# Kernel optimization log

Hardware: AMD Instinct MI355X
Metric: run time of the kernel (lower is better)

Reference implementation:

```python
import jax, jax.numpy as jnp
import numpy as np

E = 1024   # embed_dim
H = 16     # num_heads
D = E // H # head_dim = 64
HD2 = D // 2
B = 2
S = 2048


def setup_inputs() -> dict:
    key = jax.random.key(0)
    ks = jax.random.split(key, 12)
    def lin(k, fan_in, fan_out):
        # xavier-uniform-ish init, stored in [in, out] (jax) convention
        lim = float(np.sqrt(6.0 / (fan_in + fan_out)))
        return jax.random.uniform(k, (fan_in, fan_out), jnp.float32, -lim, lim)
    return {
        "query": jax.random.normal(ks[0], (B, S, E), jnp.float32),
        "xi_scale": jax.random.uniform(ks[1], (B,), jnp.float32),
        "Wq": lin(ks[2], E, E), "bq": jnp.zeros((E,), jnp.float32),
        "Wk": lin(ks[3], E, E), "bk": jnp.zeros((E,), jnp.float32),
        "Wv": lin(ks[4], E, E), "bv": jnp.zeros((E,), jnp.float32),
        "Wo": lin(ks[5], E, E), "bo": jnp.zeros((E,), jnp.float32),
        "enc_w1": lin(ks[6], 1, HD2), "enc_b1": jnp.zeros((HD2,), jnp.float32),
        "ln_g": jnp.ones((HD2,), jnp.float32), "ln_b": jnp.zeros((HD2,), jnp.float32),
        "enc_w2": lin(ks[7], HD2, D), "enc_b2": jnp.zeros((D,), jnp.float32),
        "scale_gating": jnp.ones((H,), jnp.float32),
    }


def reference(query, xi_scale, Wq, bq, Wk, bk, Wv, bv, Wo, bo,
              enc_w1, enc_b1, ln_g, ln_b, enc_w2, enc_b2, scale_gating):
    b, s, e = query.shape
    h, d = H, e // H
    # --- scale adaptation: xi -> Linear -> LayerNorm -> GELU -> Linear ---
    x = xi_scale[:, None] @ enc_w1 + enc_b1                  # [B, D/2]
    mu = x.mean(-1, keepdims=True)
    var = ((x - mu) ** 2).mean(-1, keepdims=True)
    x = (x - mu) / jnp.sqrt(var + 1e-5) * ln_g + ln_b
    x = jax.nn.gelu(x, approximate=False)
    xe = x @ enc_w2 + enc_b2                                 # [B, D]
    adapt = 1.0 + jax.nn.sigmoid(scale_gating)[None, :, None] * xe[:, None, :]  # [B, H, D]
    # --- projections (self-attention: key = value = query) ---
    q = (query @ Wq + bq).reshape(b, s, h, d).transpose(0, 2, 1, 3) * adapt[:, :, None, :]
    k = (query @ Wk + bk).reshape(b, s, h, d).transpose(0, 2, 1, 3) * adapt[:, :, None, :]
    v = (query @ Wv + bv).reshape(b, s, h, d).transpose(0, 2, 1, 3)
    # --- explicit QK^T / sqrt(d) -> softmax -> V ---
    inv_scale = 1.0 / float(np.sqrt(d))
    scores = jnp.einsum('bhqd,bhkd->bhqk', q, k) * inv_scale  # [B, H, S, S]
    attn = jax.nn.softmax(scores, axis=-1)
    out = jnp.einsum('bhqk,bhkd->bhqd', attn, v)              # [B, H, S, D]
    out = out.transpose(0, 2, 1, 3).reshape(b, s, e)
    return out @ Wo + bo
```

## Files before the change

### kernel.cpp

```cpp
#include <hip/hip_runtime.h>

typedef __bf16 bf16;
typedef __attribute__((ext_vector_type(8))) __bf16 bf16x8;
typedef __attribute__((ext_vector_type(4))) float f32x4;
typedef __attribute__((ext_vector_type(16))) float f32x16;
typedef unsigned int u32;

#define MFMA16(a, b, c) __builtin_amdgcn_mfma_f32_16x16x32_bf16((a), (b), (c), 0, 0, 0)
#define MFMA32(a, b, c) __builtin_amdgcn_mfma_f32_32x32x16_bf16((a), (b), (c), 0, 0, 0)

#define BB 2
#define SS 2048
#define EE 1024
#define HH 16
#define DD 64
#define MM (BB * SS)

__device__ inline f32x4 zero4() {
    f32x4 z; z.x = 0.f; z.y = 0.f; z.z = 0.f; z.w = 0.f; return z;
}

__device__ __forceinline__ void gload16(const bf16* g, bf16* l) {
    __builtin_amdgcn_global_load_lds(
        (const __attribute__((address_space(1))) u32*)(const void*)g,
        (__attribute__((address_space(3))) u32*)(void*)l,
        16, 0, 0);
}

__device__ __forceinline__ u32 pkbf(float a, float b) {
    union { __bf16 h; unsigned short s; } ua, ub;
    ua.h = (__bf16)a; ub.h = (__bf16)b;
    return (u32)ua.s | ((u32)ub.s << 16);
}

__global__ __launch_bounds__(256) void prep_kernel(
    const float* __restrict__ query, bf16* __restrict__ qc,
    const float* __restrict__ s0, const float* __restrict__ s1,
    const float* __restrict__ s2, const float* __restrict__ s3,
    bf16* __restrict__ d0, bf16* __restrict__ d1,
    bf16* __restrict__ d2, bf16* __restrict__ d3,
    const float* __restrict__ xi, const float* __restrict__ w1,
    const float* __restrict__ b1, const float* __restrict__ lng,
    const float* __restrict__ lnb, const float* __restrict__ w2,
    const float* __restrict__ b2, const float* __restrict__ gate,
    float* __restrict__ adapt) {
    __shared__ bf16 tile[64 * 72];
    const int bid = blockIdx.x;
    const int t = threadIdx.x;

    if (bid < 2048) {
        const int i = (bid * 256 + t) * 8;
        float4 a = *(const float4*)(query + i);
        float4 b = *(const float4*)(query + i + 4);
        bf16 tmp[8];
        tmp[0] = (bf16)a.x; tmp[1] = (bf16)a.y; tmp[2] = (bf16)a.z; tmp[3] = (bf16)a.w;
        tmp[4] = (bf16)b.x; tmp[5] = (bf16)b.y; tmp[6] = (bf16)b.z; tmp[7] = (bf16)b.w;
        *(uint4*)(qc + i) = *(uint4*)tmp;
    } else if (bid < 3072) {
        const int m = (bid - 2048) >> 8;
        const int idx0 = (bid - 2048) & 255;
        const float* W = (m == 0) ? s0 : (m == 1) ? s1 : (m == 2) ? s2 : s3;
        bf16* Wt = (m == 0) ? d0 : (m == 1) ? d1 : (m == 2) ? d2 : d3;
        const int k0 = (idx0 >> 4) * 64, n0 = (idx0 & 15) * 64;
#pragma unroll
        for (int i = 0; i < 2; ++i) {
            int idx = i * 256 + t;
            int r = idx >> 3, c = (idx & 7) * 8;
            float4 a = *(const float4*)(W + (k0 + r) * EE + n0 + c);
            float4 b = *(const float4*)(W + (k0 + r) * EE + n0 + c + 4);
            bf16 tmp[8];
            tmp[0] = (bf16)a.x; tmp[1] = (bf16)a.y; tmp[2] = (bf16)a.z; tmp[3] = (bf16)a.w;
            tmp[4] = (bf16)b.x; tmp[5] = (bf16)b.y; tmp[6] = (bf16)b.z; tmp[7] = (bf16)b.w;
            *(uint4*)(tile + r * 72 + c) = *(uint4*)tmp;
        }
        __syncthreads();
#pragma unroll
        for (int i = 0; i < 2; ++i) {
            int idx = i * 256 + t;
            int n = idx >> 3, kc = (idx & 7) * 8;
            bf16 tmp[8];
#pragma unroll
            for (int j = 0; j < 8; ++j) tmp[j] = tile[(kc + j) * 72 + n];
            *(uint4*)(Wt + (n0 + n) * EE + k0 + kc) = *(uint4*)tmp;
        }
    } else {
        const int b = bid - 3072;
        float* xs = (float*)tile;
        if (t < 64) {
            const float xiv = xi[b];
            float xv = 0.f;
            if (t < 32) xv = xiv * w1[t] + b1[t];
            float sm = xv;
            for (int off = 1; off < 32; off <<= 1) sm += __shfl_xor(sm, off);
            const float mu = sm * (1.f / 32.f);
            float dv = (t < 32) ? (xv - mu) : 0.f;
            float s2 = dv * dv;
            for (int off = 1; off < 32; off <<= 1) s2 += __shfl_xor(s2, off);
            const float var = s2 * (1.f / 32.f);
            if (t < 32) {
                float xn = (xv - mu) * rsqrtf(var + 1e-5f) * lng[t] + lnb[t];
                float ge = 0.5f * xn * (1.f + erff(xn * 0.70710678118654752f));
                xs[t] = ge;
            }
        }
        __syncthreads();
        if (t < 64) {
            float acc = b2[t];
            for (int j = 0; j < 32; ++j) acc += xs[j] * w2[j * DD + t];
            for (int h = 0; h < HH; ++h) {
                float sg = 1.f / (1.f + __expf(-gate[h]));
                adapt[(b * HH + h) * DD + t] = 1.f + sg * acc;
            }
        }
    }
}

__global__ __launch_bounds__(256, 3) void gemm_qkv(
    const bf16* __restrict__ Aq, const bf16* __restrict__ Bqk,
    const bf16* __restrict__ Av,
    const float* __restrict__ bias, const float* __restrict__ bias2,
    const float* __restrict__ bias3, const float* __restrict__ adapt,
    bf16* __restrict__ outqk, bf16* __restrict__ outvt) {
    __shared__ bf16 sh[16384];
    bf16* As = sh;
    bf16* Bs = sh + 8192;

    const int t = threadIdx.x;
    const int w = t >> 6, lane = t & 63;
    const int mrow = lane & 15, quad = lane >> 4;
    const int wm = (w & 1) * 64, wn = (w >> 1) * 64;

    int md, bx, by;
    const bf16 *Ap, *Bp;
    int bid = blockIdx.x;
    if (bid < 512) { md = 5; bx = bid & 31; by = bid >> 5; Ap = Aq; Bp = Bqk; }
    else { md = 4; bid -= 512; bx = bid & 7; by = bid >> 3; Ap = Av; Bp = Aq; }
    const int m0 = bx * 128, n0 = by * 128;
    const int m2 = (md == 5) ? (by >> 3) : 0;

    f32x4 acc[4][4];
#pragma unroll
    for (int i = 0; i < 4; ++i)
#pragma unroll
        for (int j = 0; j < 4; ++j) acc[i][j] = zero4();

    const int dr = lane >> 2;
    const int dcg = ((lane & 3) ^ (dr & 3)) * 8;
    const bf16* Ag = Ap + (size_t)(m0 + w * 16 + dr) * EE + dcg;
    const bf16* Bg = Bp + (size_t)(n0 + w * 16 + dr) * EE + dcg;
    bf16* Al = As + (w * 16) * 32;
    bf16* Bl = Bs + (w * 16) * 32;

    gload16(Ag, Al);
    gload16(Ag + 64 * EE, Al + 64 * 32);
    gload16(Bg, Bl);
    gload16(Bg + 64 * EE, Bl + 64 * 32);

    for (int kt = 0; kt < 32; ++kt) {
        __syncthreads();
        if (kt < 31) {
            const int kn = (kt + 1) * 32;
            const int nb = (kt + 1) & 1;
            gload16(Ag + kn, Al + nb * 4096);
            gload16(Ag + 64 * EE + kn, Al + nb * 4096 + 64 * 32);
            gload16(Bg + kn, Bl + nb * 4096);
            gload16(Bg + 64 * EE + kn, Bl + nb * 4096 + 64 * 32);
        }
        const bf16* Ab = As + (kt & 1) * 4096;
        const bf16* Bb = Bs + (kt & 1) * 4096;
        const int sw = (quad ^ (mrow & 3)) * 8;
        bf16x8 af[4], bfr[4];
#pragma unroll
        for (int i = 0; i < 4; ++i)
            af[i] = *(const bf16x8*)(Ab + (wm + i * 16 + mrow) * 32 + sw);
#pragma unroll
        for (int j = 0; j < 4; ++j)
            bfr[j] = *(const bf16x8*)(Bb + (wn + j * 16 + mrow) * 32 + sw);
#pragma unroll
        for (int i = 0; i < 4; ++i)
#pragma unroll
            for (int j = 0; j < 4; ++j)
                acc[i][j] = MFMA16(af[i], bfr[j], acc[i][j]);
    }

    __syncthreads();

    if (md == 5) {
        const int bq_ = m0 >> 11;
        float cmul[4], cadd[4];
#pragma unroll
        for (int j = 0; j < 4; ++j) {
            const int cl = (n0 & 1023) + wn + j * 16 + mrow;
            const int hh = cl >> 6, dd2 = cl & 63;
            const float ad = adapt[(bq_ * HH + hh) * DD + dd2];
            const float sc = m2 ? 1.f : 0.18033688011113811f;
            cmul[j] = ad * sc;
            cadd[j] = (m2 ? bias2[cl] : bias[cl]) * ad * sc;
        }
#pragma unroll
        for (int i = 0; i < 4; ++i)
#pragma unroll
            for (int j = 0; j < 4; ++j) {
                const int lcol = wn + j * 16 + mrow;
#pragma unroll
                for (int r = 0; r < 4; ++r) {
                    const int lrow = wm + i * 16 + quad * 4 + r;
                    const float v = acc[i][j][r] * cmul[j] + cadd[j];
                    *(bf16*)((char*)sh + lrow * 256 +
                             ((lcol * 2) ^ ((lrow & 15) << 4))) = (bf16)v;
                }
            }
    } else {
        float radd[16];
#pragma unroll
        for (int i = 0; i < 4; ++i)
#pragma unroll
            for (int r = 0; r < 4; ++r)
                radd[i * 4 + r] = bias3[m0 + wm + i * 16 + quad * 4 + r];
#pragma unroll
        for (int i = 0; i < 4; ++i)
#pragma unroll
            for (int j = 0; j < 4; ++j) {
                const int lcol = wn + j * 16 + mrow;
#pragma unroll
                for (int r = 0; r < 4; ++r) {
                    const int lrow = wm + i * 16 + quad * 4 + r;
                    const float v = acc[i][j][r] + radd[i * 4 + r];
                    *(bf16*)((char*)sh + lrow * 256 +
                             ((lcol * 2) ^ ((lrow & 15) << 4))) = (bf16)v;
                }
            }
    }
    __syncthreads();

#pragma unroll
    for (int p = 0; p < 8; ++p) {
        const int lrow = p * 16 + (t >> 4);
        const int lcol0 = (t & 15) * 8;
        bf16x8 val = *(const bf16x8*)((const char*)sh + lrow * 256 +
                                      ((lcol0 * 2) ^ ((lrow & 15) << 4)));
        if (md == 5) {
            const int bq_ = m0 >> 11;
            const int s_ = (m0 + lrow) & (SS - 1);
            const int cl = (n0 & 1023) + lcol0;
            const int hh = cl >> 6, d0 = cl & 63;
            if (!m2) {
                *(bf16x8*)(outqk + ((size_t)(bq_ * HH + hh) * SS + s_) * DD + d0) = val;
            } else {
                const size_t base = (size_t)MM * EE + (size_t)(bq_ * HH + hh) * 131072;
                const int a2 = (s_ >> 6) * 4096 + ((s_ >> 5) & 1) * 2048 +
                               (d0 >> 4) * 512 +
                               ((s_ & 31) + ((d0 >> 3) & 1) * 32) * 8;
                *(bf16x8*)(outqk + base + a2) = val;
            }
        } else {
            const int rowv = m0 + lrow;
            const int hv = rowv >> 6, dv = rowv & 63;
            const int colv = n0 + lcol0;
            const int bv_ = colv >> 11, sv = colv & (SS - 1);
            const size_t base = (size_t)(bv_ * HH + hv) * 131072;
            const int a2 = (sv >> 6) * 4096 + (dv >> 5) * 2048 +
                           ((sv >> 4) & 3) * 512 +
                           ((dv & 31) + ((sv >> 3) & 1) * 32) * 8;
            *(bf16x8*)(outvt + base + a2) = val;
        }
    }
}

__global__ __launch_bounds__(256, 3) void gemm_o(
    const bf16* __restrict__ A, const bf16* __restrict__ Bt,
    const float* __restrict__ bias, float* __restrict__ outf) {
    __shared__ bf16 As[2 * 128 * 64];
    __shared__ bf16 Bs[2 * 64 * 64];

    const int t = threadIdx.x;
    const int w = t >> 6, lane = t & 63;
    const int mrow = lane & 15, quad = lane >> 4;
    const int m0 = blockIdx.x * 128, n0 = blockIdx.y * 64;

    f32x4 acc[2][4];
#pragma unroll
    for (int i = 0; i < 2; ++i)
#pragma unroll
        for (int j = 0; j < 4; ++j) acc[i][j] = zero4();

    const int grow = lane >> 3;
    const int gsw = ((lane & 7) ^ grow) * 8;
    const bf16* Ag = A + (size_t)(m0 + w * 32 + grow) * EE + gsw;
    const bf16* Bg = Bt + (size_t)(n0 + w * 16 + grow) * EE + gsw;
    bf16* Al = As + (w * 32) * 64;
    bf16* Bl = Bs + (w * 16) * 64;

#pragma unroll
    for (int i = 0; i < 4; ++i) gload16(Ag + i * 8 * EE, Al + i * 8 * 64);
#pragma unroll
    for (int i = 0; i < 2; ++i) gload16(Bg + i * 8 * EE, Bl + i * 8 * 64);

    for (int kt = 0; kt < 16; ++kt) {
        __syncthreads();
        if (kt < 15) {
            const int kn = (kt + 1) * 64;
            const int nb = (kt + 1) & 1;
#pragma unroll
            for (int i = 0; i < 4; ++i)
                gload16(Ag + i * 8 * EE + kn, Al + nb * 8192 + i * 8 * 64);
#pragma unroll
            for (int i = 0; i < 2; ++i)
                gload16(Bg + i * 8 * EE + kn, Bl + nb * 4096 + i * 8 * 64);
        }
        const bf16* Ab = As + (kt & 1) * 8192;
        const bf16* Bb = Bs + (kt & 1) * 4096;
#pragma unroll
        for (int ks = 0; ks < 2; ++ks) {
            const int cg = ks * 4 + quad;
            const int sw = (cg ^ (mrow & 7)) * 8;
            bf16x8 af[2], bfr[4];
#pragma unroll
            for (int mi = 0; mi < 2; ++mi)
                af[mi] = *(const bf16x8*)(Ab + (w * 32 + mi * 16 + mrow) * 64 + sw);
#pragma unroll
            for (int nj = 0; nj < 4; ++nj)
                bfr[nj] = *(const bf16x8*)(Bb + (nj * 16 + mrow) * 64 + sw);
#pragma unroll
            for (int mi = 0; mi < 2; ++mi)
#pragma unroll
                for (int nj = 0; nj < 4; ++nj)
                    acc[mi][nj] = MFMA16(af[mi], bfr[nj], acc[mi][nj]);
        }
    }

    __syncthreads();
    char* fs = (char*)As;
    float cadd[4];
#pragma unroll
    for (int nj = 0; nj < 4; ++nj) cadd[nj] = bias[n0 + nj * 16 + mrow];
#pragma unroll
    for (int mi = 0; mi < 2; ++mi)
#pragma unroll
        for (int nj = 0; nj < 4; ++nj) {
            const int lcol = nj * 16 + mrow;
#pragma unroll
            for (int r = 0; r < 4; ++r) {
                const int lrow = w * 32 + mi * 16 + quad * 4 + r;
                *(float*)(fs + lrow * 256 + ((lcol * 4) ^ ((lrow & 15) << 4))) =
                    acc[mi][nj][r] + cadd[nj];
            }
        }
    __syncthreads();

#pragma unroll
    for (int p = 0; p < 8; ++p) {
        const int lrow = p * 16 + (t >> 4);
        const int lcol0 = (t & 15) * 4;
        float4 val = *(const float4*)(fs + lrow * 256 +
                                      ((lcol0 * 4) ^ ((lrow & 15) << 4)));
        *(float4*)(outf + (size_t)(m0 + lrow) * EE + n0 + lcol0) = val;
    }
}

__device__ __forceinline__ void attn_step(
    int kt, const bf16* kbase, const bf16* vbase,
    const bf16x8 (&qf)[4], bf16x8 (&KU)[8], bf16x8 (&KP)[8],
    f32x16 (&oacc)[2], float (&ls)[4], int h) {
    bf16x8 vf[8];
#pragma unroll
    for (int mf = 0; mf < 2; ++mf)
#pragma unroll
        for (int c = 0; c < 4; ++c)
            vf[mf * 4 + c] = *(const bf16x8*)(vbase + kt * 4096 + mf * 2048 + c * 512);

    f32x16 st[2];
#pragma unroll
    for (int mf = 0; mf < 2; ++mf)
#pragma unroll
        for (int i = 0; i < 16; ++i) st[mf][i] = 0.f;
    __builtin_amdgcn_s_setprio(1);
#pragma unroll
    for (int c = 0; c < 4; ++c)
#pragma unroll
        for (int mf = 0; mf < 2; ++mf)
            st[mf] = MFMA32(KU[mf * 4 + c], qf[c], st[mf]);
    __builtin_amdgcn_s_setprio(0);

    const int ktp = kt + (kt < SS / 64 - 1 ? 1 : 0);
#pragma unroll
    for (int mf = 0; mf < 2; ++mf)
#pragma unroll
        for (int c = 0; c < 4; ++c)
            KP[mf * 4 + c] = *(const bf16x8*)(kbase + ktp * 4096 + mf * 2048 + c * 512);

    u32 P32[2][8];
#pragma unroll
    for (int mf = 0; mf < 2; ++mf)
#pragma unroll
        for (int rp = 0; rp < 8; ++rp) {
            float pa = __builtin_amdgcn_exp2f(st[mf][2 * rp]);
            float pb = __builtin_amdgcn_exp2f(st[mf][2 * rp + 1]);
            ls[rp & 3] += pa + pb;
            P32[mf][rp] = pkbf(pa, pb);
        }

#pragma unroll
    for (int c = 0; c < 4; ++c) {
        const int mfs = c >> 1;
        const int ro = (c & 1) * 4;
        union { u32 u[4]; bf16x8 v; } pb;
        {
            u32 vA0 = P32[mfs][ro + 0], vA1 = P32[mfs][ro + 1];
            u32 vB0 = P32[mfs][ro + 2], vB1 = P32[mfs][ro + 3];
            u32 prep0 = h ? vA0 : vB0;
            u32 prep1 = h ? vA1 : vB1;
            u32 sh0 = __shfl_xor(prep0, 32);
            u32 sh1 = __shfl_xor(prep1, 32);
            pb.u[0] = h ? sh0 : vA0;
            pb.u[1] = h ? sh1 : vA1;
            pb.u[2] = h ? vB0 : sh0;
            pb.u[3] = h ? vB1 : sh1;
        }
        __builtin_amdgcn_s_setprio(1);
#pragma unroll
        for (int mf = 0; mf < 2; ++mf)
            oacc[mf] = MFMA32(vf[mf * 4 + c], pb.v, oacc[mf]);
        __builtin_amdgcn_s_setprio(0);
    }
}

__global__ __launch_bounds__(256, 2) void attn_kernel(
    const bf16* __restrict__ q, const bf16* __restrict__ k,
    const bf16* __restrict__ vt, bf16* __restrict__ o0) {
    __shared__ bf16 lds[4 * 2112];

    const int t = threadIdx.x;
    const int w = t >> 6, lane = t & 63;
    const int q32 = lane & 31, h = lane >> 5;
    const int bh = blockIdx.x & 31;
    const int qb = blockIdx.x >> 5;
    const int qr0 = qb * 128 + w * 32;

    bf16x8 qf[4];
#pragma unroll
    for (int c = 0; c < 4; ++c)
        qf[c] = *(const bf16x8*)(q + (size_t)(bh * SS + qr0 + q32) * DD + c * 16 + h * 8);

    const bf16* kbase = k + (size_t)bh * 131072 + lane * 8;
    const bf16* vbase = vt + (size_t)bh * 131072 + lane * 8;

    f32x16 oacc[2];
#pragma unroll
    for (int mf = 0; mf < 2; ++mf)
#pragma unroll
        for (int i = 0; i < 16; ++i) oacc[mf][i] = 0.f;
    float ls[4] = {0.f, 0.f, 0.f, 0.f};

    bf16x8 Ka[8], Kb[8];
#pragma unroll
    for (int mf = 0; mf < 2; ++mf)
#pragma unroll
        for (int c = 0; c < 4; ++c)
            Ka[mf * 4 + c] = *(const bf16x8*)(kbase + mf * 2048 + c * 512);

    for (int kt2 = 0; kt2 < SS / 128; ++kt2) {
        attn_step(2 * kt2,     kbase, vbase, qf, Ka, Kb, oacc, ls, h);
        attn_step(2 * kt2 + 1, kbase, vbase, qf, Kb, Ka, oacc, ls, h);
    }

    float lsum = (ls[0] + ls[1]) + (ls[2] + ls[3]);
    lsum += __shfl_xor(lsum, 32);
    const float inv = 1.f / lsum;

    bf16* ob = lds + w * 2112;
#pragma unroll
    for (int mf = 0; mf < 2; ++mf)
#pragma unroll
        for (int rp = 0; rp < 8; ++rp) {
            const int d = 32 * mf + 2 * (rp & 1) + 8 * (rp >> 1) + 4 * h;
            *(u32*)(ob + q32 * 66 + d) =
                pkbf(oacc[mf][2 * rp] * inv, oacc[mf][2 * rp + 1] * inv);
        }
    __syncthreads();

    const int b = bh >> 4, head = bh & 15;
    const int half = lane & 1;
    const int r = lane >> 1;
#pragma unroll
    for (int i = 0; i < 4; ++i) {
        bf16x8 val = *(const bf16x8*)(ob + r * 66 + half * 32 + i * 8);
        *(bf16x8*)(o0 + (size_t)(b * SS + qr0 + r) * EE + head * DD +
                   half * 32 + i * 8) = val;
    }
}

extern "C" void kernel_launch(void* const* d_in, const int* in_sizes, int n_in,
                              void* d_out, int out_size, void* d_ws, size_t ws_size,
                              hipStream_t stream) {
    const float* query = (const float*)d_in[0];
    const float* xi    = (const float*)d_in[1];
    const float* Wq = (const float*)d_in[2];  const float* bq = (const float*)d_in[3];
    const float* Wk = (const float*)d_in[4];  const float* bk = (const float*)d_in[5];
    const float* Wv = (const float*)d_in[6];  const float* bv = (const float*)d_in[7];
    const float* Wo = (const float*)d_in[8];  const float* bo = (const float*)d_in[9];
    const float* ew1 = (const float*)d_in[10]; const float* eb1 = (const float*)d_in[11];
    const float* lng = (const float*)d_in[12]; const float* lnb = (const float*)d_in[13];
    const float* ew2 = (const float*)d_in[14]; const float* eb2 = (const float*)d_in[15];
    const float* gate = (const float*)d_in[16];
    float* out = (float*)d_out;

    char* ws = (char*)d_ws;
    const size_t SZ = (size_t)MM * EE * sizeof(bf16);
    const size_t WSZ = (size_t)EE * EE * sizeof(bf16);

    bf16* queryc = (bf16*)(ws);
    bf16* p0     = (bf16*)(ws);
    bf16* qws    = (bf16*)(ws + SZ);
    bf16* kws    = (bf16*)(ws + 2 * SZ);
    bf16* vtws   = (bf16*)(ws + 3 * SZ);
    bf16* wqT    = (bf16*)(ws + 4 * SZ);
    bf16* wkT    = (bf16*)(ws + 4 * SZ + WSZ);
    bf16* wvT    = (bf16*)(ws + 4 * SZ + 2 * WSZ);
    bf16* woT    = (bf16*)(ws + 4 * SZ + 3 * WSZ);
    float* adaptws = (float*)(ws + 4 * SZ + 4 * WSZ);

    prep_kernel<<<3074, 256, 0, stream>>>(query, queryc, Wq, Wk, Wv, Wo,
                                          wqT, wkT, wvT, woT,
                                          xi, ew1, eb1, lng, lnb, ew2, eb2, gate,
                                          adaptws);

    gemm_qkv<<<768, 256, 0, stream>>>(queryc, wqT, wvT, bq, bk, bv, adaptws,
                                      qws, vtws);

    attn_kernel<<<512, 256, 0, stream>>>(qws, kws, vtws, p0);

    gemm_o<<<dim3(MM / 128, EE / 64), 256, 0, stream>>>(p0, woT, bo, out);
}
```

Before: 205.4 us.

## Software-pipeline attention: compute next tile's QK^T alongside current softmax and PV

Restructures the attention inner loop so the QK^T MFMAs for tile t+1 are issued before the exp/softmax and PV MFMAs of tile t, with K prefetched two tiles ahead. The goal is to let the matrix units stay busy while the exp and shuffle work of the current tile runs. It adds a prologue and epilogue and keeps two score accumulators live, which raises register pressure under the 2-blocks-per-CU launch bound and could cause spills.

Result: slower. 250.6 us (+22.0%).

```diff
diff --git a/kernel.cpp b/kernel.cpp
--- a/kernel.cpp
+++ b/kernel.cpp
@@ -15,6 +15,7 @@
 #define HH 16
 #define DD 64
 #define MM (BB * SS)
+#define NT (SS / 64)
 
 __device__ inline f32x4 zero4() {
     f32x4 z; z.x = 0.f; z.y = 0.f; z.z = 0.f; z.w = 0.f; return z;
@@ -358,48 +359,19 @@
     }
 }
 
-__device__ __forceinline__ void attn_step(
-    int kt, const bf16* kbase, const bf16* vbase,
-    const bf16x8 (&qf)[4], bf16x8 (&KU)[8], bf16x8 (&KP)[8],
+__device__ __forceinline__ void attn_softpv(
+    f32x16 (&stc)[2], const bf16x8 (&vf)[8],
     f32x16 (&oacc)[2], float (&ls)[4], int h) {
-    bf16x8 vf[8];
-#pragma unroll
-    for (int mf = 0; mf < 2; ++mf)
-#pragma unroll
-        for (int c = 0; c < 4; ++c)
-            vf[mf * 4 + c] = *(const bf16x8*)(vbase + kt * 4096 + mf * 2048 + c * 512);
-
-    f32x16 st[2];
-#pragma unroll
-    for (int mf = 0; mf < 2; ++mf)
-#pragma unroll
-        for (int i = 0; i < 16; ++i) st[mf][i] = 0.f;
-    __builtin_amdgcn_s_setprio(1);
-#pragma unroll
-    for (int c = 0; c < 4; ++c)
-#pragma unroll
-        for (int mf = 0; mf < 2; ++mf)
-            st[mf] = MFMA32(KU[mf * 4 + c], qf[c], st[mf]);
-    __builtin_amdgcn_s_setprio(0);
-
-    const int ktp = kt + (kt < SS / 64 - 1 ? 1 : 0);
-#pragma unroll
-    for (int mf = 0; mf < 2; ++mf)
-#pragma unroll
-        for (int c = 0; c < 4; ++c)
-            KP[mf * 4 + c] = *(const bf16x8*)(kbase + ktp * 4096 + mf * 2048 + c * 512);
-
     u32 P32[2][8];
 #pragma unroll
     for (int mf = 0; mf < 2; ++mf)
 #pragma unroll
         for (int rp = 0; rp < 8; ++rp) {
-            float pa = __builtin_amdgcn_exp2f(st[mf][2 * rp]);
-            float pb = __builtin_amdgcn_exp2f(st[mf][2 * rp + 1]);
+            float pa = __builtin_amdgcn_exp2f(stc[mf][2 * rp]);
+            float pb = __builtin_amdgcn_exp2f(stc[mf][2 * rp + 1]);
             ls[rp & 3] += pa + pb;
             P32[mf][rp] = pkbf(pa, pb);
         }
-
 #pragma unroll
     for (int c = 0; c < 4; ++c) {
         const int mfs = c >> 1;
@@ -425,6 +397,40 @@
     }
 }
 
+__device__ __forceinline__ void attn_pipe(
+    int t, const bf16* kbase, const bf16* vbase, const bf16x8 (&qf)[4],
+    f32x16 (&stc)[2], f32x16 (&stn)[2],
+    bf16x8 (&Kn)[8], bf16x8 (&Kn2)[8],
+    f32x16 (&oacc)[2], float (&ls)[4], int h) {
+    bf16x8 vf[8];
+#pragma unroll
+    for (int mf = 0; mf < 2; ++mf)
+#pragma unroll
+        for (int c = 0; c < 4; ++c)
+            vf[mf * 4 + c] = *(const bf16x8*)(vbase + t * 4096 + mf * 2048 + c * 512);
+
+    const int tk = (t + 2 < NT) ? t + 2 : NT - 1;
+#pragma unroll
+    for (int mf = 0; mf < 2; ++mf)
+#pragma unroll
+        for (int c = 0; c < 4; ++c)
+            Kn2[mf * 4 + c] = *(const bf16x8*)(kbase + tk * 4096 + mf * 2048 + c * 512);
+
+#pragma unroll
+    for (int mf = 0; mf < 2; ++mf)
+#pragma unroll
+        for (int i = 0; i < 16; ++i) stn[mf][i] = 0.f;
+    __builtin_amdgcn_s_setprio(1);
+#pragma unroll
+    for (int c = 0; c < 4; ++c)
+#pragma unroll
+        for (int mf = 0; mf < 2; ++mf)
+            stn[mf] = MFMA32(Kn[mf * 4 + c], qf[c], stn[mf]);
+    __builtin_amdgcn_s_setprio(0);
+
+    attn_softpv(stc, vf, oacc, ls, h);
+}
+
 __global__ __launch_bounds__(256, 2) void attn_kernel(
     const bf16* __restrict__ q, const bf16* __restrict__ k,
     const bf16* __restrict__ vt, bf16* __restrict__ o0) {
@@ -458,10 +464,40 @@
 #pragma unroll
         for (int c = 0; c < 4; ++c)
             Ka[mf * 4 + c] = *(const bf16x8*)(kbase + mf * 2048 + c * 512);
-
-    for (int kt2 = 0; kt2 < SS / 128; ++kt2) {
-        attn_step(2 * kt2,     kbase, vbase, qf, Ka, Kb, oacc, ls, h);
-        attn_step(2 * kt2 + 1, kbase, vbase, qf, Kb, Ka, oacc, ls, h);
+#pragma unroll
+    for (int mf = 0; mf < 2; ++mf)
+#pragma unroll
+        for (int c = 0; c < 4; ++c)
+            Kb[mf * 4 + c] = *(const bf16x8*)(kbase + 4096 + mf * 2048 + c * 512);
+
+    f32x16 stA[2], stB[2];
+#pragma unroll
+    for (int mf = 0; mf < 2; ++mf)
+#pragma unroll
+        for (int i = 0; i < 16; ++i) stA[mf][i] = 0.f;
+    __builtin_amdgcn_s_setprio(1);
+#pragma unroll
+    for (int c = 0; c < 4; ++c)
+#pragma unroll
+        for (int mf = 0; mf < 2; ++mf)
+            stA[mf] = MFMA32(Ka[mf * 4 + c], qf[c], stA[mf]);
+    __builtin_amdgcn_s_setprio(0);
+
+    for (int p = 0; p < NT / 2 - 1; ++p) {
+        attn_pipe(2 * p,     kbase, vbase, qf, stA, stB, Kb, Ka, oacc, ls, h);
+        attn_pipe(2 * p + 1, kbase, vbase, qf, stB, stA, Ka, Kb, oacc, ls, h);
+    }
+    attn_pipe(NT - 2, kbase, vbase, qf, stA, stB, Kb, Ka, oacc, ls, h);
+
+    {
+        bf16x8 vf[8];
+#pragma unroll
+        for (int mf = 0; mf < 2; ++mf)
+#pragma unroll
+            for (int c = 0; c < 4; ++c)
+                vf[mf * 4 + c] =
+                    *(const bf16x8*)(vbase + (NT - 1) * 4096 + mf * 2048 + c * 512);
+        attn_softpv(stB, vf, oacc, ls, h);
     }
 
     float lsum = (ls[0] + ls[1]) + (ls[2] + ls[3]);
```
